# Optimization experiments

Measured on AMD Instinct MI355X. Metric: run time of the kernel, lower is better.

Reference implementation:

```python
import jax, jax.numpy as jnp
import numpy as np

N_NODES = 100000
N_EDGES = 1600000
NHID = 64
NFEAT = 64
BN_EPS = 1e-5
NEG_SLOPE = 0.2  # PyG GATConv default LeakyReLU slope


def setup_inputs() -> dict:
    key = jax.random.key(0)
    ks = jax.random.split(key, 12)
    s = 0.1
    return {
        "x": jax.random.normal(ks[0], (N_NODES, NHID), jnp.float32),
        "adj": jax.random.randint(ks[1], (2, N_EDGES), 0, N_NODES, jnp.int32),
        # GATConv 1 (nhid -> nhid), single head
        "W1": jax.random.normal(ks[2], (NHID, NHID), jnp.float32) * s,
        "as1": jax.random.normal(ks[3], (NHID,), jnp.float32) * s,
        "ad1": jax.random.normal(ks[4], (NHID,), jnp.float32) * s,
        "b1": jax.random.normal(ks[5], (NHID,), jnp.float32) * s,
        # BatchNorm1d(nhid), eval mode (running stats)
        "bn_gamma": jnp.ones((NHID,), jnp.float32),
        "bn_beta": jnp.zeros((NHID,), jnp.float32),
        "bn_mean": jnp.zeros((NHID,), jnp.float32),
        "bn_var": jnp.ones((NHID,), jnp.float32),
        # GATConv 2 (nhid -> nfeat)
        "W2": jax.random.normal(ks[6], (NHID, NFEAT), jnp.float32) * s,
        "as2": jax.random.normal(ks[7], (NFEAT,), jnp.float32) * s,
        "ad2": jax.random.normal(ks[8], (NFEAT,), jnp.float32) * s,
        "b2": jax.random.normal(ks[9], (NFEAT,), jnp.float32) * s,
    }


def gat_conv(x, W, a_src_w, a_dst_w, b, src, dst, n):
    # PyG GATConv, heads=1: h = xW; e_ij = LeakyReLU(a_src.h_j + a_dst.h_i)
    # alpha = softmax over incoming edges of each dst node; out_i = sum_j alpha_ij h_j + b
    h = x @ W                                    # [N, F]
    a_src = h @ a_src_w                          # [N]
    a_dst = h @ a_dst_w                          # [N]
    e = jax.nn.leaky_relu(a_src[src] + a_dst[dst], NEG_SLOPE)  # [E]
    m = jax.ops.segment_max(e, dst, num_segments=n)
    m = jnp.where(jnp.isfinite(m), m, 0.0)
    w = jnp.exp(e - m[dst])
    s = jax.ops.segment_sum(w, dst, num_segments=n)
    alpha = w / (s[dst] + 1e-16)                 # PyG softmax eps
    out = jax.ops.segment_sum(alpha[:, None] * h[src], dst, num_segments=n)
    return out + b


def reference(x, adj, W1, as1, ad1, b1, bn_gamma, bn_beta, bn_mean, bn_var,
              W2, as2, ad2, b2):
    n = x.shape[0]
    loops = jnp.arange(n, dtype=adj.dtype)       # GATConv add_self_loops=True
    src = jnp.concatenate([adj[0], loops])
    dst = jnp.concatenate([adj[1], loops])

    h = jax.nn.relu(gat_conv(x, W1, as1, ad1, b1, src, dst, n))
    # BatchNorm1d in eval mode; dropout is identity in eval
    h = (h - bn_mean) * jax.lax.rsqrt(bn_var + BN_EPS) * bn_gamma + bn_beta
    out = jax.nn.relu(gat_conv(h, W2, as2, ad2, b2, src, dst, n))
    return out
```

## Files before the change

### kernel.cpp

```cpp
#include <hip/hip_runtime.h>
#include <math.h>

#define N_NODES 100000
#define N_EDGES 1600000
#define EP (N_EDGES + N_NODES)
#define F 64
#define NB 391
#define GR 16

__global__ __launch_bounds__(256) void k_gemm(
    const float* __restrict__ X, const float* __restrict__ W,
    const float* __restrict__ aw_s, const float* __restrict__ aw_d,
    float* __restrict__ H, float* __restrict__ asrc, float* __restrict__ adst)
{
    __shared__ float sW[64][64];
    __shared__ float sX[GR][64];
    int t = threadIdx.x;
    int r0 = blockIdx.x * GR;

    const float4* W4 = (const float4*)W;
    float4* sW4 = (float4*)sW;
#pragma unroll
    for (int i = 0; i < 4; ++i) sW4[t + i * 256] = W4[t + i * 256];
    ((float4*)sX)[t] = ((const float4*)(X + (size_t)r0 * F))[t];
    __syncthreads();

    int row = t >> 4, cg4 = (t & 15);
    float4 acc = {0.f, 0.f, 0.f, 0.f};
#pragma unroll 8
    for (int k = 0; k < 64; ++k) {
        float xv = sX[row][k];
        const float4 wv = *(const float4*)&sW[k][cg4 * 4];
        acc.x = fmaf(xv, wv.x, acc.x);
        acc.y = fmaf(xv, wv.y, acc.y);
        acc.z = fmaf(xv, wv.z, acc.z);
        acc.w = fmaf(xv, wv.w, acc.w);
    }
    ((float4*)(H + (size_t)(r0 + row) * F))[cg4] = acc;

    const float4 as4 = ((const float4*)aw_s)[cg4];
    const float4 ad4 = ((const float4*)aw_d)[cg4];
    float va = acc.x * as4.x + acc.y * as4.y + acc.z * as4.z + acc.w * as4.w;
    float vd = acc.x * ad4.x + acc.y * ad4.y + acc.z * ad4.z + acc.w * ad4.w;
#pragma unroll
    for (int off = 1; off <= 8; off <<= 1) {
        va += __shfl_xor(va, off, 64);
        vd += __shfl_xor(vd, off, 64);
    }
    if ((t & 15) == 0) { asrc[r0 + row] = va; adst[r0 + row] = vd; }
}

__global__ __launch_bounds__(256) void k_hist(
    const int* __restrict__ edst, int* __restrict__ deg, int* __restrict__ rank)
{
    int e = blockIdx.x * 256 + threadIdx.x;
    if (e >= EP) return;
    int d_ = (e < N_EDGES) ? edst[e] : e - N_EDGES;
    rank[e] = atomicAdd(deg + d_, 1);
}

__global__ __launch_bounds__(256) void k_part(
    const int* __restrict__ deg, int* __restrict__ part)
{
    __shared__ int sm[256];
    int t = threadIdx.x;
    int i = blockIdx.x * 256 + t;
    sm[t] = (i < N_NODES) ? deg[i] : 0;
    __syncthreads();
    for (int off = 128; off; off >>= 1) {
        if (t < off) sm[t] += sm[t + off];
        __syncthreads();
    }
    if (t == 0) part[blockIdx.x] = sm[0];
}

__global__ __launch_bounds__(512) void k_scanpart(
    const int* __restrict__ part, int* __restrict__ poff)
{
    __shared__ int sm[512];
    int t = threadIdx.x;
    int v = (t < NB) ? part[t] : 0;
    sm[t] = v;
    __syncthreads();
    for (int off = 1; off < 512; off <<= 1) {
        int x = (t >= off) ? sm[t - off] : 0;
        __syncthreads();
        sm[t] += x;
        __syncthreads();
    }
    if (t < NB) poff[t] = sm[t] - v;
}

__global__ __launch_bounds__(256) void k_scanfinal(
    const int* __restrict__ deg, const int* __restrict__ poff, int* __restrict__ base)
{
    __shared__ int sm[256];
    int t = threadIdx.x;
    int i = blockIdx.x * 256 + t;
    int v = (i < N_NODES) ? deg[i] : 0;
    sm[t] = v;
    __syncthreads();
    for (int off = 1; off < 256; off <<= 1) {
        int x = (t >= off) ? sm[t - off] : 0;
        __syncthreads();
        sm[t] += x;
        __syncthreads();
    }
    if (i < N_NODES) base[i] = poff[blockIdx.x] + sm[t] - v;
    if (i == 0) base[N_NODES] = EP;
}

__global__ __launch_bounds__(256) void k_scatter(
    const int* __restrict__ esrc, const int* __restrict__ edst,
    const int* __restrict__ base, const int* __restrict__ rank,
    int* __restrict__ ssrc)
{
    int e = blockIdx.x * 256 + threadIdx.x;
    if (e >= EP) return;
    int s_, d_;
    if (e < N_EDGES) { s_ = esrc[e]; d_ = edst[e]; }
    else             { s_ = d_ = e - N_EDGES; }
    ssrc[base[d_] + rank[e]] = s_;
}

template<bool BN>
__global__ __launch_bounds__(256) void k_aggr(
    const int* __restrict__ base, const int* __restrict__ ssrc,
    const float* __restrict__ asrc, const float* __restrict__ adst,
    const float* __restrict__ H, const float* __restrict__ bias,
    const float* __restrict__ gamma, const float* __restrict__ beta,
    const float* __restrict__ mean, const float* __restrict__ var,
    float* __restrict__ out)
{
    int w = threadIdx.x >> 6, lane = threadIdx.x & 63;
    int n = blockIdx.x * 4 + w;
    if (n >= N_NODES) return;
    int start = base[n], end = base[n + 1];
    float adn = adst[n];

    float mx = -1e30f;
    for (int e = start + lane; e < end; e += 64) {
        float sc = asrc[ssrc[e]] + adn;
        sc = (sc >= 0.f) ? sc : 0.2f * sc;
        mx = fmaxf(mx, sc);
    }
#pragma unroll
    for (int off = 32; off; off >>= 1) mx = fmaxf(mx, __shfl_xor(mx, off, 64));

    int g = lane >> 4, q = lane & 15;
    float4 acc = {0.f, 0.f, 0.f, 0.f};
    float ssum = 0.f;
    for (int c = start; c < end; c += 64) {
        int e = c + lane;
        bool v_ = e < end;
        int s_ = v_ ? ssrc[e] : 0;
        float sc = asrc[s_] + adn;
        sc = (sc >= 0.f) ? sc : 0.2f * sc;
        float wg = v_ ? __expf(sc - mx) : 0.f;
        ssum += wg;
        int cnt = min(64, end - c);
        for (int j = 0; j < cnt; j += 4) {
            float wj = __shfl(wg, j + g, 64);
            int   sj = __shfl(s_, j + g, 64);
            const float4 hv = *(const float4*)(H + (size_t)sj * F + q * 4);
            acc.x = fmaf(wj, hv.x, acc.x);
            acc.y = fmaf(wj, hv.y, acc.y);
            acc.z = fmaf(wj, hv.z, acc.z);
            acc.w = fmaf(wj, hv.w, acc.w);
        }
    }
#pragma unroll
    for (int off = 16; off <= 32; off <<= 1) {
        acc.x += __shfl_xor(acc.x, off, 64);
        acc.y += __shfl_xor(acc.y, off, 64);
        acc.z += __shfl_xor(acc.z, off, 64);
        acc.w += __shfl_xor(acc.w, off, 64);
    }
#pragma unroll
    for (int off = 32; off; off >>= 1) ssum += __shfl_xor(ssum, off, 64);

    if (g == 0) {
        float inv = 1.f / (ssum + 1e-16f);
        const float4 bb = ((const float4*)bias)[q];
        float4 o;
        o.x = fmaxf(fmaf(acc.x, inv, bb.x), 0.f);
        o.y = fmaxf(fmaf(acc.y, inv, bb.y), 0.f);
        o.z = fmaxf(fmaf(acc.z, inv, bb.z), 0.f);
        o.w = fmaxf(fmaf(acc.w, inv, bb.w), 0.f);
        if (BN) {
            const float4 gm = ((const float4*)gamma)[q];
            const float4 bt = ((const float4*)beta)[q];
            const float4 mn = ((const float4*)mean)[q];
            const float4 vr = ((const float4*)var)[q];
            o.x = (o.x - mn.x) * rsqrtf(vr.x + 1e-5f) * gm.x + bt.x;
            o.y = (o.y - mn.y) * rsqrtf(vr.y + 1e-5f) * gm.y + bt.y;
            o.z = (o.z - mn.z) * rsqrtf(vr.z + 1e-5f) * gm.z + bt.z;
            o.w = (o.w - mn.w) * rsqrtf(vr.w + 1e-5f) * gm.w + bt.w;
        }
        ((float4*)(out + (size_t)n * F))[q] = o;
    }
}

extern "C" void kernel_launch(void* const* d_in, const int* in_sizes, int n_in,
                              void* d_out, int out_size, void* d_ws, size_t ws_size,
                              hipStream_t stream)
{
    const float* x   = (const float*)d_in[0];
    const int*   adj = (const int*)  d_in[1];
    const float* W1  = (const float*)d_in[2];
    const float* as1 = (const float*)d_in[3];
    const float* ad1 = (const float*)d_in[4];
    const float* b1  = (const float*)d_in[5];
    const float* bng = (const float*)d_in[6];
    const float* bnb = (const float*)d_in[7];
    const float* bnm = (const float*)d_in[8];
    const float* bnv = (const float*)d_in[9];
    const float* W2  = (const float*)d_in[10];
    const float* as2 = (const float*)d_in[11];
    const float* ad2 = (const float*)d_in[12];
    const float* b2  = (const float*)d_in[13];
    float* out = (float*)d_out;

    const int* esrc = adj;
    const int* edst = adj + N_EDGES;

    float* ws   = (float*)d_ws;
    float* hA   = ws;
    float* hB   = hA + (size_t)N_NODES * F;
    float* asrc = hB + (size_t)N_NODES * F;
    float* adst = asrc + N_NODES;
    int*   deg  = (int*)(adst + N_NODES);
    int*   base = deg + N_NODES;
    int*   ssrc = base + (N_NODES + 1);
    int*   part = ssrc + EP;
    int*   poff = part + NB;
    int*   rank = (int*)hA;

    dim3 blk(256);
    int gemm_blocks = N_NODES / GR;
    int edge_blocks = (EP + 255) / 256;
    int node_blocks = (N_NODES + 3) / 4;

    hipMemsetAsync(deg, 0, N_NODES * 4, stream);
    k_hist     <<<edge_blocks, blk, 0, stream>>>(edst, deg, rank);
    k_part     <<<NB,          blk, 0, stream>>>(deg, part);
    k_scanpart <<<1,           512, 0, stream>>>(part, poff);
    k_scanfinal<<<NB,          blk, 0, stream>>>(deg, poff, base);
    k_scatter  <<<edge_blocks, blk, 0, stream>>>(esrc, edst, base, rank, ssrc);

    k_gemm        <<<gemm_blocks, blk, 0, stream>>>(x, W1, as1, ad1, hA, asrc, adst);
    k_aggr<true>  <<<node_blocks, blk, 0, stream>>>(base, ssrc, asrc, adst, hA, b1,
                                                    bng, bnb, bnm, bnv, hB);
    k_gemm        <<<gemm_blocks, blk, 0, stream>>>(hB, W2, as2, ad2, hA, asrc, adst);
    k_aggr<false> <<<node_blocks, blk, 0, stream>>>(base, ssrc, asrc, adst, hA, b2,
                                                    nullptr, nullptr, nullptr, nullptr, out);
}
```

Baseline: 397.7 us.

## Build CSR via two-level bucket sort and widen aggregation per-lane feature slice

Replaces the per-node global atomic histogram, three-pass scan and rank-based scatter with a bucketed counting sort. Edges are first histogrammed into 782 buckets of 128 nodes using shared-memory counters, then scattered as (src,dst) pairs into bucket ranges, and finally sorted within each bucket in shared memory. The aim is to cut contended global atomics and kernel launches, at the cost of an extra pass over an 8-byte-per-edge intermediate buffer. The aggregation kernel now has each lane load 8 floats of a neighbor row, processing 8 edges per step instead of 4, to raise memory-level parallelism per gather.

```diff
diff --git a/kernel.cpp b/kernel.cpp
--- a/kernel.cpp
+++ b/kernel.cpp
@@ -5,8 +5,8 @@
 #define N_EDGES 1600000
 #define EP (N_EDGES + N_NODES)
 #define F 64
-#define NB 391
 #define GR 16
+#define NBUCK 782
 
 __global__ __launch_bounds__(256) void k_gemm(
     const float* __restrict__ X, const float* __restrict__ W,
@@ -50,77 +50,89 @@
     if ((t & 15) == 0) { asrc[r0 + row] = va; adst[r0 + row] = vd; }
 }
 
-__global__ __launch_bounds__(256) void k_hist(
-    const int* __restrict__ edst, int* __restrict__ deg, int* __restrict__ rank)
-{
-    int e = blockIdx.x * 256 + threadIdx.x;
-    if (e >= EP) return;
-    int d_ = (e < N_EDGES) ? edst[e] : e - N_EDGES;
-    rank[e] = atomicAdd(deg + d_, 1);
-}
-
-__global__ __launch_bounds__(256) void k_part(
-    const int* __restrict__ deg, int* __restrict__ part)
-{
-    __shared__ int sm[256];
-    int t = threadIdx.x;
-    int i = blockIdx.x * 256 + t;
-    sm[t] = (i < N_NODES) ? deg[i] : 0;
-    __syncthreads();
-    for (int off = 128; off; off >>= 1) {
-        if (t < off) sm[t] += sm[t + off];
-        __syncthreads();
-    }
-    if (t == 0) part[blockIdx.x] = sm[0];
-}
-
-__global__ __launch_bounds__(512) void k_scanpart(
-    const int* __restrict__ part, int* __restrict__ poff)
-{
-    __shared__ int sm[512];
-    int t = threadIdx.x;
-    int v = (t < NB) ? part[t] : 0;
+__global__ __launch_bounds__(256) void k_bhist(
+    const int* __restrict__ edst, int* __restrict__ bcount)
+{
+    __shared__ int h[NBUCK];
+    int t = threadIdx.x;
+    for (int i = t; i < NBUCK; i += 256) h[i] = 0;
+    __syncthreads();
+    for (int e = blockIdx.x * 256 + t; e < EP; e += gridDim.x * 256) {
+        int d_ = (e < N_EDGES) ? edst[e] : e - N_EDGES;
+        atomicAdd(&h[d_ >> 7], 1);
+    }
+    __syncthreads();
+    for (int i = t; i < NBUCK; i += 256)
+        if (h[i]) atomicAdd(&bcount[i], h[i]);
+}
+
+__global__ __launch_bounds__(1024) void k_bscan(
+    const int* __restrict__ bcount, int* __restrict__ bbase,
+    int* __restrict__ bcursor, int* __restrict__ base)
+{
+    __shared__ int sm[1024];
+    int t = threadIdx.x;
+    int v = (t < NBUCK) ? bcount[t] : 0;
     sm[t] = v;
     __syncthreads();
-    for (int off = 1; off < 512; off <<= 1) {
+    for (int off = 1; off < 1024; off <<= 1) {
         int x = (t >= off) ? sm[t - off] : 0;
         __syncthreads();
         sm[t] += x;
         __syncthreads();
     }
-    if (t < NB) poff[t] = sm[t] - v;
-}
-
-__global__ __launch_bounds__(256) void k_scanfinal(
-    const int* __restrict__ deg, const int* __restrict__ poff, int* __restrict__ base)
-{
-    __shared__ int sm[256];
-    int t = threadIdx.x;
-    int i = blockIdx.x * 256 + t;
-    int v = (i < N_NODES) ? deg[i] : 0;
-    sm[t] = v;
-    __syncthreads();
-    for (int off = 1; off < 256; off <<= 1) {
-        int x = (t >= off) ? sm[t - off] : 0;
-        __syncthreads();
-        sm[t] += x;
-        __syncthreads();
-    }
-    if (i < N_NODES) base[i] = poff[blockIdx.x] + sm[t] - v;
-    if (i == 0) base[N_NODES] = EP;
-}
-
-__global__ __launch_bounds__(256) void k_scatter(
+    if (t < NBUCK) { int ex = sm[t] - v; bbase[t] = ex; bcursor[t] = ex; }
+    if (t == 0) { bbase[NBUCK] = EP; base[N_NODES] = EP; }
+}
+
+__global__ __launch_bounds__(256) void k_bscatter(
     const int* __restrict__ esrc, const int* __restrict__ edst,
-    const int* __restrict__ base, const int* __restrict__ rank,
-    int* __restrict__ ssrc)
+    int* __restrict__ bcursor, int2* __restrict__ ebuf)
 {
     int e = blockIdx.x * 256 + threadIdx.x;
     if (e >= EP) return;
     int s_, d_;
     if (e < N_EDGES) { s_ = esrc[e]; d_ = edst[e]; }
     else             { s_ = d_ = e - N_EDGES; }
-    ssrc[base[d_] + rank[e]] = s_;
+    int p = atomicAdd(&bcursor[d_ >> 7], 1);
+    ebuf[p] = make_int2(s_, d_);
+}
+
+__global__ __launch_bounds__(256) void k_bucket(
+    const int2* __restrict__ ebuf, const int* __restrict__ bbase,
+    int* __restrict__ base, int* __restrict__ ssrc)
+{
+    __shared__ int deg[128], sc[128], cur[128];
+    int t = threadIdx.x;
+    int b = blockIdx.x;
+    int nb0 = b << 7;
+    int lo = bbase[b], hi = bbase[b + 1];
+
+    if (t < 128) deg[t] = 0;
+    __syncthreads();
+    for (int i = lo + t; i < hi; i += 256)
+        atomicAdd(&deg[ebuf[i].y - nb0], 1);
+    __syncthreads();
+    if (t < 128) sc[t] = deg[t];
+    __syncthreads();
+    for (int off = 1; off < 128; off <<= 1) {
+        int x = (t < 128 && t >= off) ? sc[t - off] : 0;
+        __syncthreads();
+        if (t < 128) sc[t] += x;
+        __syncthreads();
+    }
+    if (t < 128) {
+        int ex = lo + sc[t] - deg[t];
+        cur[t] = ex;
+        int n = nb0 + t;
+        if (n < N_NODES) base[n] = ex;
+    }
+    __syncthreads();
+    for (int i = lo + t; i < hi; i += 256) {
+        int2 e = ebuf[i];
+        int p = atomicAdd(&cur[e.y - nb0], 1);
+        ssrc[p] = e.x;
+    }
 }
 
 template<bool BN>
@@ -147,8 +159,8 @@
 #pragma unroll
     for (int off = 32; off; off >>= 1) mx = fmaxf(mx, __shfl_xor(mx, off, 64));
 
-    int g = lane >> 4, q = lane & 15;
-    float4 acc = {0.f, 0.f, 0.f, 0.f};
+    int g = lane >> 3, q = lane & 7;
+    float4 aLo = {0.f, 0.f, 0.f, 0.f}, aHi = {0.f, 0.f, 0.f, 0.f};
     float ssum = 0.f;
     for (int c = start; c < end; c += 64) {
         int e = c + lane;
@@ -159,45 +171,66 @@
         float wg = v_ ? __expf(sc - mx) : 0.f;
         ssum += wg;
         int cnt = min(64, end - c);
-        for (int j = 0; j < cnt; j += 4) {
+        for (int j = 0; j < cnt; j += 8) {
             float wj = __shfl(wg, j + g, 64);
             int   sj = __shfl(s_, j + g, 64);
-            const float4 hv = *(const float4*)(H + (size_t)sj * F + q * 4);
-            acc.x = fmaf(wj, hv.x, acc.x);
-            acc.y = fmaf(wj, hv.y, acc.y);
-            acc.z = fmaf(wj, hv.z, acc.z);
-            acc.w = fmaf(wj, hv.w, acc.w);
+            const float4* hp = (const float4*)(H + (size_t)sj * F + q * 8);
+            const float4 h0 = hp[0];
+            const float4 h1 = hp[1];
+            aLo.x = fmaf(wj, h0.x, aLo.x);
+            aLo.y = fmaf(wj, h0.y, aLo.y);
+            aLo.z = fmaf(wj, h0.z, aLo.z);
+            aLo.w = fmaf(wj, h0.w, aLo.w);
+            aHi.x = fmaf(wj, h1.x, aHi.x);
+            aHi.y = fmaf(wj, h1.y, aHi.y);
+            aHi.z = fmaf(wj, h1.z, aHi.z);
+            aHi.w = fmaf(wj, h1.w, aHi.w);
         }
     }
 #pragma unroll
-    for (int off = 16; off <= 32; off <<= 1) {
-        acc.x += __shfl_xor(acc.x, off, 64);
-        acc.y += __shfl_xor(acc.y, off, 64);
-        acc.z += __shfl_xor(acc.z, off, 64);
-        acc.w += __shfl_xor(acc.w, off, 64);
+    for (int off = 8; off <= 32; off <<= 1) {
+        aLo.x += __shfl_xor(aLo.x, off, 64);
+        aLo.y += __shfl_xor(aLo.y, off, 64);
+        aLo.z += __shfl_xor(aLo.z, off, 64);
+        aLo.w += __shfl_xor(aLo.w, off, 64);
+        aHi.x += __shfl_xor(aHi.x, off, 64);
+        aHi.y += __shfl_xor(aHi.y, off, 64);
+        aHi.z += __shfl_xor(aHi.z, off, 64);
+        aHi.w += __shfl_xor(aHi.w, off, 64);
     }
 #pragma unroll
     for (int off = 32; off; off >>= 1) ssum += __shfl_xor(ssum, off, 64);
 
     if (g == 0) {
         float inv = 1.f / (ssum + 1e-16f);
-        const float4 bb = ((const float4*)bias)[q];
-        float4 o;
-        o.x = fmaxf(fmaf(acc.x, inv, bb.x), 0.f);
-        o.y = fmaxf(fmaf(acc.y, inv, bb.y), 0.f);
-        o.z = fmaxf(fmaf(acc.z, inv, bb.z), 0.f);
-        o.w = fmaxf(fmaf(acc.w, inv, bb.w), 0.f);
+        const float4 bL = ((const float4*)bias)[q * 2];
+        const float4 bH = ((const float4*)bias)[q * 2 + 1];
+        float4 oL, oH;
+        oL.x = fmaxf(fmaf(aLo.x, inv, bL.x), 0.f);
+        oL.y = fmaxf(fmaf(aLo.y, inv, bL.y), 0.f);
+        oL.z = fmaxf(fmaf(aLo.z, inv, bL.z), 0.f);
+        oL.w = fmaxf(fmaf(aLo.w, inv, bL.w), 0.f);
+        oH.x = fmaxf(fmaf(aHi.x, inv, bH.x), 0.f);
+        oH.y = fmaxf(fmaf(aHi.y, inv, bH.y), 0.f);
+        oH.z = fmaxf(fmaf(aHi.z, inv, bH.z), 0.f);
+        oH.w = fmaxf(fmaf(aHi.w, inv, bH.w), 0.f);
         if (BN) {
-            const float4 gm = ((const float4*)gamma)[q];
-            const float4 bt = ((const float4*)beta)[q];
-            const float4 mn = ((const float4*)mean)[q];
-            const float4 vr = ((const float4*)var)[q];
-            o.x = (o.x - mn.x) * rsqrtf(vr.x + 1e-5f) * gm.x + bt.x;
-            o.y = (o.y - mn.y) * rsqrtf(vr.y + 1e-5f) * gm.y + bt.y;
-            o.z = (o.z - mn.z) * rsqrtf(vr.z + 1e-5f) * gm.z + bt.z;
-            o.w = (o.w - mn.w) * rsqrtf(vr.w + 1e-5f) * gm.w + bt.w;
+            const float4 gL = ((const float4*)gamma)[q*2], gH = ((const float4*)gamma)[q*2+1];
+            const float4 tL = ((const float4*)beta)[q*2],  tH = ((const float4*)beta)[q*2+1];
+            const float4 mL = ((const float4*)mean)[q*2],  mH = ((const float4*)mean)[q*2+1];
+            const float4 vL = ((const float4*)var)[q*2],   vH = ((const float4*)var)[q*2+1];
+            oL.x = (oL.x - mL.x) * rsqrtf(vL.x + 1e-5f) * gL.x + tL.x;
+            oL.y = (oL.y - mL.y) * rsqrtf(vL.y + 1e-5f) * gL.y + tL.y;
+            oL.z = (oL.z - mL.z) * rsqrtf(vL.z + 1e-5f) * gL.z + tL.z;
+            oL.w = (oL.w - mL.w) * rsqrtf(vL.w + 1e-5f) * gL.w + tL.w;
+            oH.x = (oH.x - mH.x) * rsqrtf(vH.x + 1e-5f) * gH.x + tH.x;
+            oH.y = (oH.y - mH.y) * rsqrtf(vH.y + 1e-5f) * gH.y + tH.y;
+            oH.z = (oH.z - mH.z) * rsqrtf(vH.z + 1e-5f) * gH.z + tH.z;
+            oH.w = (oH.w - mH.w) * rsqrtf(vH.w + 1e-5f) * gH.w + tH.w;
         }
-        ((float4*)(out + (size_t)n * F))[q] = o;
+        float4* op = (float4*)(out + (size_t)n * F);
+        op[q * 2]     = oL;
+        op[q * 2 + 1] = oH;
     }
 }
 
@@ -229,24 +262,23 @@
     float* hB   = hA + (size_t)N_NODES * F;
     float* asrc = hB + (size_t)N_NODES * F;
     float* adst = asrc + N_NODES;
-    int*   deg  = (int*)(adst + N_NODES);
-    int*   base = deg + N_NODES;
+    int*   base = (int*)(adst + N_NODES);
     int*   ssrc = base + (N_NODES + 1);
-    int*   part = ssrc + EP;
-    int*   poff = part + NB;
-    int*   rank = (int*)hA;
+    int*   bcount  = ssrc + EP;
+    int*   bbase   = bcount + NBUCK;
+    int*   bcursor = bbase + NBUCK + 1;
+    int2*  ebuf = (int2*)hA;
 
     dim3 blk(256);
     int gemm_blocks = N_NODES / GR;
     int edge_blocks = (EP + 255) / 256;
     int node_blocks = (N_NODES + 3) / 4;
 
-    hipMemsetAsync(deg, 0, N_NODES * 4, stream);
-    k_hist     <<<edge_blocks, blk, 0, stream>>>(edst, deg, rank);
-    k_part     <<<NB,          blk, 0, stream>>>(deg, part);
-    k_scanpart <<<1,           512, 0, stream>>>(part, poff);
-    k_scanfinal<<<NB,          blk, 0, stream>>>(deg, poff, base);
-    k_scatter  <<<edge_blocks, blk, 0, stream>>>(esrc, edst, base, rank, ssrc);
+    hipMemsetAsync(bcount, 0, NBUCK * 4, stream);
+    k_bhist    <<<512,         blk, 0, stream>>>(edst, bcount);
+    k_bscan    <<<1,          1024, 0, stream>>>(bcount, bbase, bcursor, base);
+    k_bscatter <<<edge_blocks, blk, 0, stream>>>(esrc, edst, bcursor, ebuf);
+    k_bucket   <<<NBUCK,       blk, 0, stream>>>(ebuf, bbase, base, ssrc);
 
     k_gemm        <<<gemm_blocks, blk, 0, stream>>>(x, W1, as1, ad1, hA, asrc, adst);
     k_aggr<true>  <<<node_blocks, blk, 0, stream>>>(base, ssrc, asrc, adst, hA, b1,
```

Measured after the change: 765.1 us. 1.92x slower.
